# Kernel tuning notes

Measured on AMD Instinct MI355X. Metric: run time of the kernel, lower is better.

The kernel has to match this reference:

```python
import jax, jax.numpy as jnp
import numpy as np

VOCAB = 256
D = 512
L = 2
FFN = 2048
H = 8
HD = D // H  # head dim = random-feature dim m for favor+
B = 2
T = 2048


def setup_inputs() -> dict:
    key = jax.random.key(0)
    ks = jax.random.split(key, 16)
    rng = np.random.default_rng(0)

    def lin(k, fan_in, shape):
        return jax.random.normal(k, shape, jnp.float32) / np.sqrt(fan_in)

    tokens = jax.random.randint(ks[0], (B, T), 0, VOCAB)
    emb = jax.random.normal(ks[1], (VOCAB, D // 2), jnp.float32)
    Wq = lin(ks[2], D, (L, D, D)); bq = 0.01 * jax.random.normal(ks[3], (L, D), jnp.float32)
    Wk = lin(ks[4], D, (L, D, D)); bk = 0.01 * jax.random.normal(ks[5], (L, D), jnp.float32)
    Wv = lin(ks[6], D, (L, D, D)); bv = 0.01 * jax.random.normal(ks[7], (L, D), jnp.float32)
    WU = lin(ks[8], D, (L, D, FFN)); bU = 0.01 * jax.random.normal(ks[9], (L, FFN), jnp.float32)
    WV = lin(ks[10], FFN, (L, FFN, D)); bV = 0.01 * jax.random.normal(ks[11], (L, D), jnp.float32)
    Wout = lin(ks[12], D, (D, VOCAB)); bout = 0.01 * jax.random.normal(ks[13], (VOCAB,), jnp.float32)
    ln1_g = jnp.ones((L, D), jnp.float32) + 0.02 * jax.random.normal(ks[14], (L, D), jnp.float32)
    ln2_g = jnp.ones((L, D), jnp.float32) + 0.02 * jax.random.normal(ks[15], (L, D), jnp.float32)
    ln1_b = jnp.zeros((L, D), jnp.float32)
    ln2_b = jnp.zeros((L, D), jnp.float32)
    # orthogonal random features per (layer, head), scaled by sqrt(head_dim)
    rfs_np = np.stack([
        np.stack([np.linalg.qr(rng.standard_normal((HD, HD)))[0] * np.sqrt(HD) for _ in range(H)])
        for _ in range(L)
    ]).astype(np.float32)
    rfs = jnp.asarray(rfs_np)
    return dict(tokens=tokens, emb=emb, Wq=Wq, bq=bq, Wk=Wk, bk=bk, Wv=Wv, bv=bv,
                rfs=rfs, ln1_g=ln1_g, ln1_b=ln1_b, ln2_g=ln2_g, ln2_b=ln2_b,
                WU=WU, bU=bU, WV=WV, bV=bV, Wout=Wout, bout=bout)


def _layernorm(x, g, b, eps=1e-5):
    mu = jnp.mean(x, -1, keepdims=True)
    var = jnp.mean((x - mu) ** 2, -1, keepdims=True)
    return (x - mu) * jax.lax.rsqrt(var + eps) * g + b


def _favor_feat(x, rfs):
    # x: [B,T,H,d]; rfs: [H,d,m]
    xp = x * (HD ** -0.25)
    return jnp.exp(jnp.einsum('bthd,hdm->bthm', xp, rfs)
                   - 0.5 * jnp.sum(xp ** 2, -1, keepdims=True))


def _attention(x, Wq, bq, Wk, bk, Wv, bv, rfs):
    Bx, Tx, Dm = x.shape
    q = (x @ Wq + bq).reshape(Bx, Tx, H, HD)
    k = (x @ Wk + bk).reshape(Bx, Tx, H, HD)
    v = (x @ Wv + bv).reshape(Bx, Tx, H, HD)
    qf = _favor_feat(q, rfs)  # [B,T,H,m]
    kf = _favor_feat(k, rfs)
    # causal prefix-sum (num_ps / den_ps with zero init sums)
    kv_cum = jnp.cumsum(jnp.einsum('bthm,bthd->bthmd', kf, v), axis=1)
    num = jnp.einsum('bthm,bthmd->bthd', qf, kv_cum)
    den = jnp.einsum('bthm,bthm->bth', qf, jnp.cumsum(kf, axis=1))
    return (num / (den[..., None] + 1e-16)).reshape(Bx, Tx, Dm)


def _pos_embs(x):
    # x: [B,T,D//2]; concat fixed sinusoidal embeddings of size D//2
    Bx, Tx, half = x.shape
    positions = jnp.arange(Tx, dtype=x.dtype)
    freqs = jnp.exp(jnp.arange(0, half, 2, dtype=x.dtype) * (-np.log(10000.0) / half))
    args = positions[:, None] * freqs[None, :]  # [T, half//2]
    sin = jnp.broadcast_to(jnp.sin(args)[None], (Bx, Tx, args.shape[1]))
    cos = jnp.broadcast_to(jnp.cos(args)[None], (Bx, Tx, args.shape[1]))
    return jnp.concatenate([x, sin, cos], -1)


def reference(tokens, emb, Wq, bq, Wk, bk, Wv, bv, rfs,
              ln1_g, ln1_b, ln2_g, ln2_b, WU, bU, WV, bV, Wout, bout):
    x = emb[tokens]            # [B,T,D//2]
    x = _pos_embs(x)           # [B,T,D]
    for i in range(L):
        skip = x
        a = _attention(x, Wq[i], bq[i], Wk[i], bk[i], Wv[i], bv[i], rfs[i])
        a = _layernorm(a, ln1_g[i], ln1_b[i])  # on_gptln=True: LN after attention
        x = skip + a
        skip = x
        h = jax.nn.gelu(x @ WU[i] + bU[i], approximate=False)
        h = h @ WV[i] + bV[i]
        h = _layernorm(h, ln2_g[i], ln2_b[i])  # on_gptln=True: LN after FFN
        x = skip + h
    return x @ Wout + bout     # [B,T,VOCAB]
```

## Files before the change

### kernel.cpp

```cpp
#include <hip/hip_runtime.h>
#include <hip/hip_bf16.h>
#include <math.h>

#define B_  2
#define T_  2048
#define D_  512
#define H_  8
#define HD_ 64
#define FFN_ 2048
#define VOCAB_ 256
#define BT_ (B_*T_)
#define NC_ 32
#define CENT_ 4160

typedef __attribute__((ext_vector_type(8))) short short8;
typedef __attribute__((ext_vector_type(4))) float float4v;
typedef __hip_bfloat16 bf16;

__device__ __forceinline__ void load16_lds(const void* g, void* l) {
  __builtin_amdgcn_global_load_lds(
      (const __attribute__((address_space(1))) unsigned int*)g,
      (__attribute__((address_space(3))) unsigned int*)l,
      16, 0, 0);
}

__device__ __forceinline__ unsigned short f2bf(float f) {
  bf16 h = __float2bfloat16(f);
  return __builtin_bit_cast(unsigned short, h);
}
__device__ __forceinline__ float bf2f(unsigned short u) {
  unsigned int i = ((unsigned int)u) << 16;
  return __builtin_bit_cast(float, i);
}

__global__ __launch_bounds__(512) void embed_pos_kernel(
    const int* __restrict__ tokens, const float* __restrict__ emb,
    float* __restrict__ x, bf16* __restrict__ xb)
{
  int bt = blockIdx.x;
  int t  = bt & (T_ - 1);
  int j  = threadIdx.x;
  float val;
  if (j < 256) {
    int tok = tokens[bt];
    val = emb[tok * 256 + j];
  } else {
    int jj = (j - 256) & 127;
    float f = expf(-(float)(2 * jj) * (9.210340371976184f / 256.0f));
    float arg = (float)t * f;
    val = (j < 384) ? sinf(arg) : cosf(arg);
  }
  size_t off = (size_t)bt * D_ + j;
  x[off]  = val;
  xb[off] = __float2bfloat16(val);
}

__global__ __launch_bounds__(256) void prep_all_kernel(
    const float* __restrict__ Wv, const float* __restrict__ WU,
    const float* __restrict__ WVp, const float* __restrict__ Wout,
    bf16* __restrict__ WvT, bf16* __restrict__ WUT,
    bf16* __restrict__ WVT, bf16* __restrict__ WoutT,
    const float* __restrict__ bq, const float* __restrict__ bk,
    const float* __restrict__ rfs, float* __restrict__ bqf,
    float* __restrict__ bkf)
{
  __shared__ float t[32][33];
  int id = blockIdx.x;
  if (id >= 4736) {
    int z = id - 4736;
    int l = z >> 1, side = z & 1;
    const float* b = (side ? bk : bq) + l * D_;
    float* bo = (side ? bkf : bqf) + l * D_;
    for (int n = threadIdx.x; n < D_; n += 256) {
      int h = n >> 6, j = n & 63;
      const float* R = rfs + ((size_t)l * H_ + h) * 4096;
      float acc = 0.f;
      for (int d = 0; d < 64; ++d) acc += b[h * 64 + d] * R[d * 64 + j];
      bo[n] = acc * 0.35355339059327373f;
    }
    return;
  }
  const float* W; bf16* Wt; int K, N, tx, ty;
  if (id < 512) {
    int l = id >> 8, tt = id & 255;
    W = Wv + (size_t)l * D_ * D_;  Wt = WvT + (size_t)l * D_ * D_;
    K = D_; N = D_; tx = tt & 15; ty = tt >> 4;
  } else if (id < 2560) {
    int tt = id - 512; int l = tt >> 10; tt &= 1023;
    W = WU + (size_t)l * D_ * FFN_;  Wt = WUT + (size_t)l * D_ * FFN_;
    K = D_; N = FFN_; tx = tt & 63; ty = tt >> 6;
  } else if (id < 4608) {
    int tt = id - 2560; int l = tt >> 10; tt &= 1023;
    W = WVp + (size_t)l * FFN_ * D_;  Wt = WVT + (size_t)l * FFN_ * D_;
    K = FFN_; N = D_; tx = tt & 15; ty = tt >> 4;
  } else {
    int tt = id - 4608;
    W = Wout;  Wt = WoutT;
    K = D_; N = VOCAB_; tx = tt & 7; ty = tt >> 3;
  }
  int n0 = tx * 32, k0 = ty * 32;
  int lx = threadIdx.x & 31, ly = threadIdx.x >> 5;
#pragma unroll
  for (int r = 0; r < 4; ++r)
    t[ly + 8 * r][lx] = W[(size_t)(k0 + ly + 8 * r) * N + n0 + lx];
  __syncthreads();
#pragma unroll
  for (int r = 0; r < 4; ++r)
    Wt[(size_t)(n0 + ly + 8 * r) * K + k0 + lx] = __float2bfloat16(t[lx][ly + 8 * r]);
}

__global__ __launch_bounds__(256) void rf_fold_w_kernel(
    const float* __restrict__ Wq, const float* __restrict__ Wk,
    const float* __restrict__ rfs, bf16* __restrict__ WqT, bf16* __restrict__ WkT)
{
  int h = blockIdx.x, kq = blockIdx.y, z = blockIdx.z;
  int l = z >> 1, side = z & 1;
  const float* W = (side ? Wk : Wq) + (size_t)l * D_ * D_;
  bf16* WT = (side ? WkT : WqT) + (size_t)l * D_ * D_;
  const float* Rg = rfs + ((size_t)l * H_ + h) * 4096;
  __shared__ float Rl[64][65];
  __shared__ float Ws[128][65];
  int tid = threadIdx.x;
  for (int i = tid; i < 1024; i += 256) {
    float4 v4 = ((const float4*)Rg)[i];
    int d = i >> 4, j0 = (i & 15) * 4;
    Rl[d][j0] = v4.x; Rl[d][j0+1] = v4.y; Rl[d][j0+2] = v4.z; Rl[d][j0+3] = v4.w;
  }
  for (int i = tid; i < 2048; i += 256) {
    int r = i >> 4, c0 = (i & 15) * 4;
    float4 v4 = *(const float4*)&W[(size_t)(kq * 128 + r) * D_ + h * 64 + c0];
    Ws[r][c0] = v4.x; Ws[r][c0+1] = v4.y; Ws[r][c0+2] = v4.z; Ws[r][c0+3] = v4.w;
  }
  __syncthreads();
  int lane = tid & 63, w = tid >> 6;
  for (int kh = 0; kh < 2; ++kh) {
    int kk = kh * 64 + lane;
#pragma unroll 1
    for (int jj = 0; jj < 16; ++jj) {
      int j = w * 16 + jj;
      float acc = 0.f;
#pragma unroll 16
      for (int d = 0; d < 64; ++d) acc += Ws[kk][d] * Rl[d][j];
      WT[(size_t)(h * 64 + j) * D_ + kq * 128 + kk] =
          __float2bfloat16(acc * 0.35355339059327373f);
    }
  }
}

__device__ __forceinline__ void mfma_core(
    const bf16* __restrict__ A, const bf16* __restrict__ Bt,
    int strideK, int kr, int row0, int col0, float4v acc[4][4])
{
  __shared__ short Al[128 * 64];
  __shared__ short Bl[128 * 64];
  int tid = threadIdx.x;
  int lane = tid & 63, w = tid >> 6;
  int wm = (w >> 1) * 64, wn = (w & 1) * 64;
  int quad = lane >> 4, l16 = lane & 15;

  int lr = lane >> 3;
  int ks = (((lane & 7) ^ lr)) * 8;
  const short* gA[4]; const short* gB[4];
  short* lA[4]; short* lB[4];
#pragma unroll
  for (int p = 0; p < 4; ++p) {
    int r = 32 * w + 8 * p;
    gA[p] = (const short*)A + (size_t)(row0 + r + lr) * strideK + ks;
    gB[p] = (const short*)Bt + (size_t)(col0 + r + lr) * strideK + ks;
    lA[p] = Al + r * 64;
    lB[p] = Bl + r * 64;
  }
#pragma unroll
  for (int p = 0; p < 4; ++p) {
    load16_lds(gA[p], lA[p]);
    load16_lds(gB[p], lB[p]);
  }

  for (int kt = 0; kt < kr; ++kt) {
    __syncthreads();
    short8 af[4][2], bfr[4][2];
#pragma unroll
    for (int mi = 0; mi < 4; ++mi) {
      int R = wm + mi * 16 + l16;
#pragma unroll
      for (int s = 0; s < 2; ++s) {
        int slot = (s * 4 + quad) ^ (R & 7);
        af[mi][s] = *(const short8*)&Al[R * 64 + slot * 8];
      }
    }
#pragma unroll
    for (int ni = 0; ni < 4; ++ni) {
      int R = wn + ni * 16 + l16;
#pragma unroll
      for (int s = 0; s < 2; ++s) {
        int slot = (s * 4 + quad) ^ (R & 7);
        bfr[ni][s] = *(const short8*)&Bl[R * 64 + slot * 8];
      }
    }
    __syncthreads();
    if (kt + 1 < kr) {
      int o = (kt + 1) * 64;
#pragma unroll
      for (int p = 0; p < 4; ++p) {
        load16_lds(gA[p] + o, lA[p]);
        load16_lds(gB[p] + o, lB[p]);
      }
    }
#pragma unroll
    for (int mi = 0; mi < 4; ++mi)
#pragma unroll
      for (int ni = 0; ni < 4; ++ni) {
        acc[mi][ni] = __builtin_amdgcn_mfma_f32_16x16x32_bf16(
            af[mi][0], bfr[ni][0], acc[mi][ni], 0, 0, 0);
        acc[mi][ni] = __builtin_amdgcn_mfma_f32_16x16x32_bf16(
            af[mi][1], bfr[ni][1], acc[mi][ni], 0, 0, 0);
      }
  }
}

__global__ __launch_bounds__(256) void gemm_mfma(
    const bf16* __restrict__ A, const bf16* __restrict__ Bt,
    const float* __restrict__ bias, void* __restrict__ Cout,
    int M, int N, int K, int mode)
{
  int lane = threadIdx.x & 63, w = threadIdx.x >> 6;
  int wm = (w >> 1) * 64, wn = (w & 1) * 64;
  int quad = lane >> 4, l16 = lane & 15;
  int row0 = blockIdx.x * 128, col0 = blockIdx.y * 128;
  float4v acc[4][4] = {};
  mfma_core(A, Bt, K, K >> 6, row0, col0, acc);
#pragma unroll
  for (int mi = 0; mi < 4; ++mi) {
#pragma unroll
    for (int ni = 0; ni < 4; ++ni) {
      int j = col0 + wn + ni * 16 + l16;
      float bj = bias[j];
#pragma unroll
      for (int r = 0; r < 4; ++r) {
        int i = row0 + wm + mi * 16 + quad * 4 + r;
        float v = acc[mi][ni][r] + bj;
        if (mode == 1) {
          v = 0.5f * v * (1.0f + erff(v * 0.7071067811865475f));
          ((bf16*)Cout)[(size_t)i * N + j] = __float2bfloat16(v);
        } else {
          ((float*)Cout)[(size_t)i * N + j] = v;
        }
      }
    }
  }
}

__global__ __launch_bounds__(256) void gemm_qkv(
    const bf16* __restrict__ A, const bf16* __restrict__ wT,
    const float* __restrict__ bqf, const float* __restrict__ bkf,
    const float* __restrict__ bv, bf16* __restrict__ outb, int l)
{
  int z = blockIdx.z;
  const bf16* Bt = wT + ((size_t)z * 2 + l) * D_ * D_;
  const float* bias = (z == 0 ? bqf : (z == 1 ? bkf : bv)) + l * D_;
  bf16* Cout = outb + (size_t)z * BT_ * D_;
  int lane = threadIdx.x & 63, w = threadIdx.x >> 6;
  int wm = (w >> 1) * 64, wn = (w & 1) * 64;
  int quad = lane >> 4, l16 = lane & 15;
  int row0 = blockIdx.x * 128, col0 = blockIdx.y * 128;
  float4v acc[4][4] = {};
  mfma_core(A, Bt, D_, D_ >> 6, row0, col0, acc);
  if (z < 2) {
#pragma unroll
    for (int mi = 0; mi < 4; ++mi) {
      float vres[4][4];
      float sq[4] = {0.f, 0.f, 0.f, 0.f};
#pragma unroll
      for (int ni = 0; ni < 4; ++ni) {
        int j = col0 + wn + ni * 16 + l16;
        float bj = bias[j];
#pragma unroll
        for (int r = 0; r < 4; ++r) {
          float v = acc[mi][ni][r] + bj;
          vres[ni][r] = v;
          sq[r] += v * v;
        }
      }
#pragma unroll
      for (int r = 0; r < 4; ++r) {
        float s = sq[r];
        s += __shfl_xor(s, 1, 64);
        s += __shfl_xor(s, 2, 64);
        s += __shfl_xor(s, 4, 64);
        s += __shfl_xor(s, 8, 64);
        sq[r] = s;
      }
#pragma unroll
      for (int ni = 0; ni < 4; ++ni) {
        int j = col0 + wn + ni * 16 + l16;
#pragma unroll
        for (int r = 0; r < 4; ++r) {
          int i = row0 + wm + mi * 16 + quad * 4 + r;
          Cout[(size_t)i * D_ + j] =
              __float2bfloat16(__expf(vres[ni][r] - sq[r] * (1.0f / 128.0f)));
        }
      }
    }
  } else {
#pragma unroll
    for (int mi = 0; mi < 4; ++mi) {
#pragma unroll
      for (int ni = 0; ni < 4; ++ni) {
        int j = col0 + wn + ni * 16 + l16;
        float bj = bias[j];
#pragma unroll
        for (int r = 0; r < 4; ++r) {
          int i = row0 + wm + mi * 16 + quad * 4 + r;
          Cout[(size_t)i * D_ + j] = __float2bfloat16(acc[mi][ni][r] + bj);
        }
      }
    }
  }
}

__global__ __launch_bounds__(256) void gemm_splitk(
    const bf16* __restrict__ A, const bf16* __restrict__ Bt,
    float* __restrict__ P, int M, int N, int K, int KS)
{
  int s = blockIdx.z;
  int lane = threadIdx.x & 63, w = threadIdx.x >> 6;
  int wm = (w >> 1) * 64, wn = (w & 1) * 64;
  int quad = lane >> 4, l16 = lane & 15;
  int row0 = blockIdx.x * 128, col0 = blockIdx.y * 128;
  float4v acc[4][4] = {};
  mfma_core((const bf16*)((const short*)A + s * KS),
            (const bf16*)((const short*)Bt + s * KS),
            K, KS >> 6, row0, col0, acc);
  float* Ps = P + (size_t)s * M * N;
#pragma unroll
  for (int mi = 0; mi < 4; ++mi) {
#pragma unroll
    for (int ni = 0; ni < 4; ++ni) {
      int j = col0 + wn + ni * 16 + l16;
#pragma unroll
      for (int r = 0; r < 4; ++r) {
        int i = row0 + wm + mi * 16 + quad * 4 + r;
        Ps[(size_t)i * N + j] = acc[mi][ni][r];
      }
    }
  }
}

__global__ __launch_bounds__(256) void reduce4_bias_kernel(
    const float* __restrict__ P, const float* __restrict__ bias,
    float* __restrict__ C, int MN, int N)
{
  int idx = (blockIdx.x * 256 + threadIdx.x) * 4;
  float4 s0 = *(const float4*)&P[idx];
  float4 s1 = *(const float4*)&P[idx + MN];
  float4 s2 = *(const float4*)&P[idx + 2 * MN];
  float4 s3 = *(const float4*)&P[idx + 3 * MN];
  float4 b  = *(const float4*)&bias[idx & (N - 1)];
  float4 r;
  r.x = s0.x + s1.x + s2.x + s3.x + b.x;
  r.y = s0.y + s1.y + s2.y + s3.y + b.y;
  r.z = s0.z + s1.z + s2.z + s3.z + b.z;
  r.w = s0.w + s1.w + s2.w + s3.w + b.w;
  *(float4*)&C[idx] = r;
}

__global__ __launch_bounds__(256) void reduce_ln_add_kernel(
    const float* __restrict__ P, const float* __restrict__ bias,
    float* __restrict__ x, bf16* __restrict__ xb,
    const float* __restrict__ g, const float* __restrict__ bta)
{
  const int MN = BT_ * D_;
  int row = blockIdx.x;
  int tid = threadIdx.x;
  size_t base = (size_t)row * D_;
  float v0 = P[base + tid] + P[MN + base + tid] + P[2 * MN + base + tid]
           + P[3 * MN + base + tid] + bias[tid];
  float v1 = P[base + tid + 256] + P[MN + base + tid + 256]
           + P[2 * MN + base + tid + 256] + P[3 * MN + base + tid + 256]
           + bias[tid + 256];
  __shared__ float red[4];
  float w = v0 + v1;
  for (int o = 32; o > 0; o >>= 1) w += __shfl_down(w, o, 64);
  if ((tid & 63) == 0) red[tid >> 6] = w;
  __syncthreads();
  float mu = (red[0] + red[1] + red[2] + red[3]) * (1.f / 512.f);
  float d0 = v0 - mu, d1 = v1 - mu;
  __syncthreads();
  w = d0 * d0 + d1 * d1;
  for (int o = 32; o > 0; o >>= 1) w += __shfl_down(w, o, 64);
  if ((tid & 63) == 0) red[tid >> 6] = w;
  __syncthreads();
  float var = (red[0] + red[1] + red[2] + red[3]) * (1.f / 512.f);
  float rs = rsqrtf(var + 1e-5f);
  float n0 = x[base + tid]       + d0 * rs * g[tid]       + bta[tid];
  float n1 = x[base + tid + 256] + d1 * rs * g[tid + 256] + bta[tid + 256];
  x[base + tid]        = n0;
  x[base + tid + 256]  = n1;
  xb[base + tid]       = __float2bfloat16(n0);
  xb[base + tid + 256] = __float2bfloat16(n1);
}

__global__ __launch_bounds__(256) void chunk_sum_kernel(
    const bf16* __restrict__ kf, const bf16* __restrict__ vf,
    float* __restrict__ buf)
{
  int bh = blockIdx.x / 31;
  int c  = blockIdx.x % 31;
  int b = bh >> 3, h = bh & 7;
  __shared__ short KT[64 * 64];
  __shared__ short VT[64 * 64];
  __shared__ float zpart[4][64];
  int tid = threadIdx.x;
  int m = tid & 63, g = tid >> 6;
  const size_t rowbase = ((size_t)(b * T_ + c * 64)) * D_ + h * 64;
#pragma unroll
  for (int cc0 = 0; cc0 < 2; ++cc0) {
    int cc = g + cc0 * 4;
    short8 kk, vv;
#pragma unroll
    for (int u = 0; u < 8; ++u) {
      size_t off = rowbase + (size_t)(cc * 8 + u) * D_ + m;
      kk[u] = ((const short*)kf)[off];
      vv[u] = ((const short*)vf)[off];
    }
    int slot = cc ^ (m & 7);
    *(short8*)&KT[m * 64 + slot * 8] = kk;
    *(short8*)&VT[m * 64 + slot * 8] = vv;
  }
  __syncthreads();
  int quad = (tid & 63) >> 4, l16 = tid & 15;
  int ar = g * 16 + l16;
  short8 afr[2];
#pragma unroll
  for (int s = 0; s < 2; ++s)
    afr[s] = *(const short8*)&KT[ar * 64 + ((s * 4 + quad) ^ (ar & 7)) * 8];
  float4v acc[4] = {};
#pragma unroll
  for (int nd = 0; nd < 4; ++nd) {
    int br = nd * 16 + l16;
#pragma unroll
    for (int s = 0; s < 2; ++s) {
      short8 bfr = *(const short8*)&VT[br * 64 + ((s * 4 + quad) ^ (br & 7)) * 8];
      acc[nd] = __builtin_amdgcn_mfma_f32_16x16x32_bf16(afr[s], bfr, acc[nd], 0, 0, 0);
    }
  }
  float zp = 0.f;
#pragma unroll
  for (int cc0 = 0; cc0 < 2; ++cc0) {
    int cc = g + cc0 * 4;
    short8 kk = *(const short8*)&KT[m * 64 + (cc ^ (m & 7)) * 8];
#pragma unroll
    for (int u = 0; u < 8; ++u) zp += bf2f((unsigned short)kk[u]);
  }
  zpart[g][m] = zp;
  size_t bo = (size_t)(bh * 31 + c) * CENT_;
#pragma unroll
  for (int nd = 0; nd < 4; ++nd)
#pragma unroll
    for (int r = 0; r < 4; ++r)
      buf[bo + (size_t)(g * 16 + quad * 4 + r) * 64 + nd * 16 + l16] = acc[nd][r];
  __syncthreads();
  if (tid < 64)
    buf[bo + 4096 + tid] = zpart[0][tid] + zpart[1][tid] + zpart[2][tid] + zpart[3][tid];
}

__global__ __launch_bounds__(256) void chunk_prefix_kernel(float* __restrict__ buf)
{
  int bh = blockIdx.x / 17;
  int grp = blockIdx.x % 17;
  int e = grp * 256 + threadIdx.x;
  if (e >= CENT_) return;
  size_t base = (size_t)bh * 31 * CENT_ + e;
  float vals[31];
#pragma unroll
  for (int c = 0; c < 31; ++c) vals[c] = buf[base + (size_t)c * CENT_];
  float run = 0.f;
#pragma unroll
  for (int c = 0; c < 31; ++c) {
    run += vals[c];
    buf[base + (size_t)c * CENT_] = run;
  }
}

__global__ __launch_bounds__(256) void chunk_attn_kernel(
    const bf16* __restrict__ qf, const bf16* __restrict__ kf,
    const bf16* __restrict__ vf, const float* __restrict__ buf,
    float* __restrict__ out)
{
  int bh = blockIdx.x >> 5;
  int ck = blockIdx.x & 31;
  int b = bh >> 3, h = bh & 7;
  __shared__ short Qs[64 * 64];
  __shared__ short Ks[64 * 64];
  __shared__ short VT[64 * 64];
  __shared__ short S0T[64 * 64];
  __shared__ float z0[64];
  __shared__ float dlds[64];
  __shared__ float dpartA[64];
  __shared__ float dpartQ[4][64];
  int tid = threadIdx.x;
  int lane = tid & 63, w = tid >> 6;
  int quad = lane >> 4, l16 = lane & 15;
  const size_t rb = ((size_t)(b * T_ + ck * 64)) * D_ + h * 64;

  {
    int lr = lane >> 3;
    int fc = (lane & 7) ^ lr;
#pragma unroll
    for (int seg = 0; seg < 2; ++seg) {
      int r = 16 * w + 8 * seg;
      load16_lds((const short*)qf + rb + (size_t)(r + lr) * D_ + fc * 8, &Qs[r * 64]);
      load16_lds((const short*)kf + rb + (size_t)(r + lr) * D_ + fc * 8, &Ks[r * 64]);
    }
    int d = lane;
    const float* S0 = buf + (size_t)(bh * 31 + (ck > 0 ? ck - 1 : 0)) * CENT_;
#pragma unroll
    for (int cc0 = 0; cc0 < 2; ++cc0) {
      int cc = w + cc0 * 4;
      short8 vv, ss;
#pragma unroll
      for (int u = 0; u < 8; ++u) {
        vv[u] = ((const short*)vf)[rb + (size_t)(cc * 8 + u) * D_ + d];
        ss[u] = (ck > 0) ? (short)f2bf(S0[(size_t)(cc * 8 + u) * 64 + d]) : (short)0;
      }
      int slot = cc ^ (d & 7);
      *(short8*)&VT[d * 64 + slot * 8] = vv;
      *(short8*)&S0T[d * 64 + slot * 8] = ss;
    }
    if (tid < 64) z0[tid] = (ck > 0) ? S0[4096 + tid] : 0.f;
  }
  __syncthreads();

  float4v pacc[4] = {};
  {
    int ar = 16 * w + l16;
    short8 afr[2];
#pragma unroll
    for (int s = 0; s < 2; ++s)
      afr[s] = *(const short8*)&Qs[ar * 64 + ((s * 4 + quad) ^ (ar & 7)) * 8];
#pragma unroll
    for (int nj = 0; nj < 4; ++nj) {
      int br = nj * 16 + l16;
#pragma unroll
      for (int s = 0; s < 2; ++s) {
        short8 bfr = *(const short8*)&Ks[br * 64 + ((s * 4 + quad) ^ (br & 7)) * 8];
        pacc[nj] = __builtin_amdgcn_mfma_f32_16x16x32_bf16(afr[s], bfr, pacc[nj], 0, 0, 0);
      }
    }
  }
  {
    int i = lane;
    float qz = 0.f;
#pragma unroll
    for (int cc0 = 0; cc0 < 2; ++cc0) {
      int cc = w + cc0 * 4;
      short8 qq = *(const short8*)&Qs[i * 64 + (cc ^ (i & 7)) * 8];
#pragma unroll
      for (int u = 0; u < 8; ++u) qz += bf2f((unsigned short)qq[u]) * z0[cc * 8 + u];
    }
    dpartQ[w][i] = qz;
  }
  __syncthreads();

  {
    float rs[4] = {0.f, 0.f, 0.f, 0.f};
#pragma unroll
    for (int nj = 0; nj < 4; ++nj) {
#pragma unroll
      for (int r = 0; r < 4; ++r) {
        int i = 16 * w + quad * 4 + r;
        int j = nj * 16 + l16;
        float val = (j <= i) ? pacc[nj][r] : 0.f;
        rs[r] += val;
        ((unsigned short*)Ks)[i * 64 + ((j >> 3) ^ (i & 7)) * 8 + (j & 7)] = f2bf(val);
      }
    }
#pragma unroll
    for (int r = 0; r < 4; ++r) {
      float s = rs[r];
      s += __shfl_xor(s, 1, 64);
      s += __shfl_xor(s, 2, 64);
      s += __shfl_xor(s, 4, 64);
      s += __shfl_xor(s, 8, 64);
      rs[r] = s;
    }
    if (l16 == 0) {
#pragma unroll
      for (int r = 0; r < 4; ++r) dpartA[16 * w + quad * 4 + r] = rs[r];
    }
  }
  __syncthreads();
  if (tid < 64)
    dlds[tid] = dpartA[tid] + dpartQ[0][tid] + dpartQ[1][tid]
              + dpartQ[2][tid] + dpartQ[3][tid];

  float4v acc[4] = {};
  {
    int ar = 16 * w + l16;
    short8 aA[2], aQ[2];
#pragma unroll
    for (int s = 0; s < 2; ++s) {
      aA[s] = *(const short8*)&Ks[ar * 64 + ((s * 4 + quad) ^ (ar & 7)) * 8];
      aQ[s] = *(const short8*)&Qs[ar * 64 + ((s * 4 + quad) ^ (ar & 7)) * 8];
    }
#pragma unroll
    for (int nd = 0; nd < 4; ++nd) {
      int br = nd * 16 + l16;
#pragma unroll
      for (int s = 0; s < 2; ++s) {
        short8 bV = *(const short8*)&VT[br * 64 + ((s * 4 + quad) ^ (br & 7)) * 8];
        acc[nd] = __builtin_amdgcn_mfma_f32_16x16x32_bf16(aA[s], bV, acc[nd], 0, 0, 0);
        short8 bS = *(const short8*)&S0T[br * 64 + ((s * 4 + quad) ^ (br & 7)) * 8];
        acc[nd] = __builtin_amdgcn_mfma_f32_16x16x32_bf16(aQ[s], bS, acc[nd], 0, 0, 0);
      }
    }
  }
  __syncthreads();
#pragma unroll
  for (int nd = 0; nd < 4; ++nd)
#pragma unroll
    for (int r = 0; r < 4; ++r) {
      int i = 16 * w + quad * 4 + r;
      int d = nd * 16 + l16;
      out[((size_t)(b * T_ + ck * 64 + i)) * D_ + h * 64 + d] =
          acc[nd][r] / (dlds[i] + 1e-16f);
    }
}

__global__ __launch_bounds__(256) void ln_add_kernel(
    float* __restrict__ x, bf16* __restrict__ xb, const float* __restrict__ a,
    const float* __restrict__ g, const float* __restrict__ bta)
{
  int row = blockIdx.x;
  int tid = threadIdx.x;
  const float* ar = a + (size_t)row * D_;
  float v0 = ar[tid], v1 = ar[tid + 256];
  __shared__ float red[4];
  float w = v0 + v1;
  for (int o = 32; o > 0; o >>= 1) w += __shfl_down(w, o, 64);
  if ((tid & 63) == 0) red[tid >> 6] = w;
  __syncthreads();
  float mu = (red[0] + red[1] + red[2] + red[3]) * (1.f / 512.f);
  float d0 = v0 - mu, d1 = v1 - mu;
  __syncthreads();
  w = d0 * d0 + d1 * d1;
  for (int o = 32; o > 0; o >>= 1) w += __shfl_down(w, o, 64);
  if ((tid & 63) == 0) red[tid >> 6] = w;
  __syncthreads();
  float var = (red[0] + red[1] + red[2] + red[3]) * (1.f / 512.f);
  float rs = rsqrtf(var + 1e-5f);
  size_t xoff = (size_t)row * D_;
  float n0 = x[xoff + tid]       + d0 * rs * g[tid]       + bta[tid];
  float n1 = x[xoff + tid + 256] + d1 * rs * g[tid + 256] + bta[tid + 256];
  x[xoff + tid]        = n0;
  x[xoff + tid + 256]  = n1;
  xb[xoff + tid]       = __float2bfloat16(n0);
  xb[xoff + tid + 256] = __float2bfloat16(n1);
}

extern "C" void kernel_launch(void* const* d_in, const int* in_sizes, int n_in,
                              void* d_out, int out_size, void* d_ws, size_t ws_size,
                              hipStream_t stream) {
  const int*   tokens = (const int*)  d_in[0];
  const float* emb    = (const float*)d_in[1];
  const float* Wq     = (const float*)d_in[2];
  const float* bq     = (const float*)d_in[3];
  const float* Wk     = (const float*)d_in[4];
  const float* bk     = (const float*)d_in[5];
  const float* Wv     = (const float*)d_in[6];
  const float* bv     = (const float*)d_in[7];
  const float* rfs    = (const float*)d_in[8];
  const float* ln1g   = (const float*)d_in[9];
  const float* ln1b   = (const float*)d_in[10];
  const float* ln2g   = (const float*)d_in[11];
  const float* ln2b   = (const float*)d_in[12];
  const float* WU     = (const float*)d_in[13];
  const float* bU     = (const float*)d_in[14];
  const float* WV     = (const float*)d_in[15];
  const float* bV     = (const float*)d_in[16];
  const float* Wout   = (const float*)d_in[17];
  const float* bout   = (const float*)d_in[18];
  float* out = (float*)d_out;

  const size_t R = (size_t)BT_ * D_;
  float* ws = (float*)d_ws;
  float* x  = ws;
  float* ab = ws + R;
  float* sb = ws + 2 * R;
  bf16*  qb = (bf16*)(ws + 3 * R);
  bf16*  kb = (bf16*)(ws + 3 * R + R / 2);
  bf16*  vb = (bf16*)(ws + 4 * R);
  bf16*  xb = (bf16*)(ws + 4 * R + R / 2);
  bf16*  hb = (bf16*)(ws + 5 * R);
  float* pb = ws + 7 * R;
  bf16*  wT = (bf16*)(ws + 11 * R);
  bf16* WqT   = wT;
  bf16* WkT   = WqT + (size_t)2 * D_ * D_;
  bf16* WvT   = WkT + (size_t)2 * D_ * D_;
  bf16* WUT   = WvT + (size_t)2 * D_ * D_;
  bf16* WVT   = WUT + (size_t)2 * D_ * FFN_;
  bf16* WoutT = WVT + (size_t)2 * D_ * FFN_;
  float* bqf  = (float*)(WoutT + (size_t)VOCAB_ * D_);
  float* bkf  = bqf + 2 * D_;

  rf_fold_w_kernel<<<dim3(8, 4, 4), 256, 0, stream>>>(Wq, Wk, rfs, WqT, WkT);
  prep_all_kernel<<<4740, 256, 0, stream>>>(
      Wv, WU, WV, Wout, WvT, WUT, WVT, WoutT, bq, bk, rfs, bqf, bkf);

  embed_pos_kernel<<<BT_, 512, 0, stream>>>(tokens, emb, x, xb);

  for (int l = 0; l < 2; ++l) {
    gemm_qkv<<<dim3(BT_/128, D_/128, 3), 256, 0, stream>>>(
        xb, wT, bqf, bkf, bv, qb, l);

    chunk_sum_kernel<<<16 * 31, 256, 0, stream>>>(kb, vb, sb);
    chunk_prefix_kernel<<<16 * 17, 256, 0, stream>>>(sb);
    chunk_attn_kernel<<<16 * NC_, 256, 0, stream>>>(qb, kb, vb, sb, ab);

    ln_add_kernel<<<BT_, 256, 0, stream>>>(x, xb, ab, ln1g + l*D_, ln1b + l*D_);

    gemm_mfma<<<dim3(BT_/128, FFN_/128), 256, 0, stream>>>(
        xb, WUT + (size_t)l*D_*FFN_, bU + l*FFN_, hb, BT_, FFN_, D_, 1);

    gemm_splitk<<<dim3(BT_/128, D_/128, 4), 256, 0, stream>>>(
        hb, WVT + (size_t)l*FFN_*D_, pb, BT_, D_, FFN_, FFN_/4);
    reduce_ln_add_kernel<<<BT_, 256, 0, stream>>>(
        pb, bV + l*D_, x, xb, ln2g + l*D_, ln2b + l*D_);
  }

  gemm_splitk<<<dim3(BT_/128, VOCAB_/128, 4), 256, 0, stream>>>(
      xb, WoutT, pb, BT_, VOCAB_, D_, D_/4);
  reduce4_bias_kernel<<<(BT_*VOCAB_)/1024, 256, 0, stream>>>(
      pb, bout, out, BT_*VOCAB_, VOCAB_);
}
```

Before: 320.9 us.

## Merge prologue kernels into one launch and double GEMM K-tile to 128

New measurement: 354.5 us. +10.4%, slower.

```diff
diff --git a/kernel.cpp b/kernel.cpp
--- a/kernel.cpp
+++ b/kernel.cpp
@@ -33,117 +33,126 @@
   return __builtin_bit_cast(float, i);
 }
 
-__global__ __launch_bounds__(512) void embed_pos_kernel(
+__global__ __launch_bounds__(256) void prologue_kernel(
     const int* __restrict__ tokens, const float* __restrict__ emb,
-    float* __restrict__ x, bf16* __restrict__ xb)
-{
-  int bt = blockIdx.x;
-  int t  = bt & (T_ - 1);
-  int j  = threadIdx.x;
-  float val;
-  if (j < 256) {
-    int tok = tokens[bt];
-    val = emb[tok * 256 + j];
-  } else {
-    int jj = (j - 256) & 127;
-    float f = expf(-(float)(2 * jj) * (9.210340371976184f / 256.0f));
-    float arg = (float)t * f;
-    val = (j < 384) ? sinf(arg) : cosf(arg);
-  }
-  size_t off = (size_t)bt * D_ + j;
-  x[off]  = val;
-  xb[off] = __float2bfloat16(val);
-}
-
-__global__ __launch_bounds__(256) void prep_all_kernel(
+    float* __restrict__ x, bf16* __restrict__ xb,
+    const float* __restrict__ Wq, const float* __restrict__ Wk,
+    const float* __restrict__ rfs, bf16* __restrict__ WqT, bf16* __restrict__ WkT,
     const float* __restrict__ Wv, const float* __restrict__ WU,
     const float* __restrict__ WVp, const float* __restrict__ Wout,
     bf16* __restrict__ WvT, bf16* __restrict__ WUT,
     bf16* __restrict__ WVT, bf16* __restrict__ WoutT,
     const float* __restrict__ bq, const float* __restrict__ bk,
-    const float* __restrict__ rfs, float* __restrict__ bqf,
-    float* __restrict__ bkf)
-{
-  __shared__ float t[32][33];
+    float* __restrict__ bqf, float* __restrict__ bkf)
+{
+  __shared__ float sm[12480];
   int id = blockIdx.x;
-  if (id >= 4736) {
-    int z = id - 4736;
+  int tid = threadIdx.x;
+
+  if (id < 4096) {
+    int bt = id;
+    int t  = bt & (T_ - 1);
+#pragma unroll
+    for (int jj = 0; jj < 2; ++jj) {
+      int j = tid + jj * 256;
+      float val;
+      if (j < 256) {
+        int tok = tokens[bt];
+        val = emb[tok * 256 + j];
+      } else {
+        int j2 = (j - 256) & 127;
+        float f = expf(-(float)(2 * j2) * (9.210340371976184f / 256.0f));
+        float arg = (float)t * f;
+        val = (j < 384) ? sinf(arg) : cosf(arg);
+      }
+      size_t off = (size_t)bt * D_ + j;
+      x[off]  = val;
+      xb[off] = __float2bfloat16(val);
+    }
+    return;
+  }
+  if (id < 4224) {
+    int id2 = id - 4096;
+    int h = id2 & 7, kq = (id2 >> 3) & 3, z = id2 >> 5;
+    int l = z >> 1, side = z & 1;
+    const float* W = (side ? Wk : Wq) + (size_t)l * D_ * D_;
+    bf16* WT = (side ? WkT : WqT) + (size_t)l * D_ * D_;
+    const float* Rg = rfs + ((size_t)l * H_ + h) * 4096;
+    float* Rl = sm;
+    float* Ws = sm + 64 * 65;
+    for (int i = tid; i < 1024; i += 256) {
+      float4 v4 = ((const float4*)Rg)[i];
+      int d = i >> 4, j0 = (i & 15) * 4;
+      Rl[d * 65 + j0] = v4.x; Rl[d * 65 + j0 + 1] = v4.y;
+      Rl[d * 65 + j0 + 2] = v4.z; Rl[d * 65 + j0 + 3] = v4.w;
+    }
+    for (int i = tid; i < 2048; i += 256) {
+      int r = i >> 4, c0 = (i & 15) * 4;
+      float4 v4 = *(const float4*)&W[(size_t)(kq * 128 + r) * D_ + h * 64 + c0];
+      Ws[r * 65 + c0] = v4.x; Ws[r * 65 + c0 + 1] = v4.y;
+      Ws[r * 65 + c0 + 2] = v4.z; Ws[r * 65 + c0 + 3] = v4.w;
+    }
+    __syncthreads();
+    int lane = tid & 63, w = tid >> 6;
+    for (int kh = 0; kh < 2; ++kh) {
+      int kk = kh * 64 + lane;
+#pragma unroll 1
+      for (int jj = 0; jj < 16; ++jj) {
+        int j = w * 16 + jj;
+        float acc = 0.f;
+#pragma unroll 16
+        for (int d = 0; d < 64; ++d) acc += Ws[kk * 65 + d] * Rl[d * 65 + j];
+        WT[(size_t)(h * 64 + j) * D_ + kq * 128 + kk] =
+            __float2bfloat16(acc * 0.35355339059327373f);
+      }
+    }
+    return;
+  }
+  if (id < 8960) {
+    int id3 = id - 4224;
+    const float* W; bf16* Wt; int K, N, tx, ty;
+    if (id3 < 512) {
+      int l = id3 >> 8, tt = id3 & 255;
+      W = Wv + (size_t)l * D_ * D_;  Wt = WvT + (size_t)l * D_ * D_;
+      K = D_; N = D_; tx = tt & 15; ty = tt >> 4;
+    } else if (id3 < 2560) {
+      int tt = id3 - 512; int l = tt >> 10; tt &= 1023;
+      W = WU + (size_t)l * D_ * FFN_;  Wt = WUT + (size_t)l * D_ * FFN_;
+      K = D_; N = FFN_; tx = tt & 63; ty = tt >> 6;
+    } else if (id3 < 4608) {
+      int tt = id3 - 2560; int l = tt >> 10; tt &= 1023;
+      W = WVp + (size_t)l * FFN_ * D_;  Wt = WVT + (size_t)l * FFN_ * D_;
+      K = FFN_; N = D_; tx = tt & 15; ty = tt >> 4;
+    } else {
+      int tt = id3 - 4608;
+      W = Wout;  Wt = WoutT;
+      K = D_; N = VOCAB_; tx = tt & 7; ty = tt >> 3;
+    }
+    float (*tb)[33] = (float(*)[33])sm;
+    int n0 = tx * 32, k0 = ty * 32;
+    int lx = tid & 31, ly = tid >> 5;
+#pragma unroll
+    for (int r = 0; r < 4; ++r)
+      tb[ly + 8 * r][lx] = W[(size_t)(k0 + ly + 8 * r) * N + n0 + lx];
+    __syncthreads();
+#pragma unroll
+    for (int r = 0; r < 4; ++r)
+      Wt[(size_t)(n0 + ly + 8 * r) * K + k0 + lx] =
+          __float2bfloat16(tb[lx][ly + 8 * r]);
+    return;
+  }
+  {
+    int z = id - 8960;
     int l = z >> 1, side = z & 1;
     const float* b = (side ? bk : bq) + l * D_;
     float* bo = (side ? bkf : bqf) + l * D_;
-    for (int n = threadIdx.x; n < D_; n += 256) {
+    for (int n = tid; n < D_; n += 256) {
       int h = n >> 6, j = n & 63;
       const float* R = rfs + ((size_t)l * H_ + h) * 4096;
       float acc = 0.f;
       for (int d = 0; d < 64; ++d) acc += b[h * 64 + d] * R[d * 64 + j];
       bo[n] = acc * 0.35355339059327373f;
     }
-    return;
-  }
-  const float* W; bf16* Wt; int K, N, tx, ty;
-  if (id < 512) {
-    int l = id >> 8, tt = id & 255;
-    W = Wv + (size_t)l * D_ * D_;  Wt = WvT + (size_t)l * D_ * D_;
-    K = D_; N = D_; tx = tt & 15; ty = tt >> 4;
-  } else if (id < 2560) {
-    int tt = id - 512; int l = tt >> 10; tt &= 1023;
-    W = WU + (size_t)l * D_ * FFN_;  Wt = WUT + (size_t)l * D_ * FFN_;
-    K = D_; N = FFN_; tx = tt & 63; ty = tt >> 6;
-  } else if (id < 4608) {
-    int tt = id - 2560; int l = tt >> 10; tt &= 1023;
-    W = WVp + (size_t)l * FFN_ * D_;  Wt = WVT + (size_t)l * FFN_ * D_;
-    K = FFN_; N = D_; tx = tt & 15; ty = tt >> 4;
-  } else {
-    int tt = id - 4608;
-    W = Wout;  Wt = WoutT;
-    K = D_; N = VOCAB_; tx = tt & 7; ty = tt >> 3;
-  }
-  int n0 = tx * 32, k0 = ty * 32;
-  int lx = threadIdx.x & 31, ly = threadIdx.x >> 5;
-#pragma unroll
-  for (int r = 0; r < 4; ++r)
-    t[ly + 8 * r][lx] = W[(size_t)(k0 + ly + 8 * r) * N + n0 + lx];
-  __syncthreads();
-#pragma unroll
-  for (int r = 0; r < 4; ++r)
-    Wt[(size_t)(n0 + ly + 8 * r) * K + k0 + lx] = __float2bfloat16(t[lx][ly + 8 * r]);
-}
-
-__global__ __launch_bounds__(256) void rf_fold_w_kernel(
-    const float* __restrict__ Wq, const float* __restrict__ Wk,
-    const float* __restrict__ rfs, bf16* __restrict__ WqT, bf16* __restrict__ WkT)
-{
-  int h = blockIdx.x, kq = blockIdx.y, z = blockIdx.z;
-  int l = z >> 1, side = z & 1;
-  const float* W = (side ? Wk : Wq) + (size_t)l * D_ * D_;
-  bf16* WT = (side ? WkT : WqT) + (size_t)l * D_ * D_;
-  const float* Rg = rfs + ((size_t)l * H_ + h) * 4096;
-  __shared__ float Rl[64][65];
-  __shared__ float Ws[128][65];
-  int tid = threadIdx.x;
-  for (int i = tid; i < 1024; i += 256) {
-    float4 v4 = ((const float4*)Rg)[i];
-    int d = i >> 4, j0 = (i & 15) * 4;
-    Rl[d][j0] = v4.x; Rl[d][j0+1] = v4.y; Rl[d][j0+2] = v4.z; Rl[d][j0+3] = v4.w;
-  }
-  for (int i = tid; i < 2048; i += 256) {
-    int r = i >> 4, c0 = (i & 15) * 4;
-    float4 v4 = *(const float4*)&W[(size_t)(kq * 128 + r) * D_ + h * 64 + c0];
-    Ws[r][c0] = v4.x; Ws[r][c0+1] = v4.y; Ws[r][c0+2] = v4.z; Ws[r][c0+3] = v4.w;
-  }
-  __syncthreads();
-  int lane = tid & 63, w = tid >> 6;
-  for (int kh = 0; kh < 2; ++kh) {
-    int kk = kh * 64 + lane;
-#pragma unroll 1
-    for (int jj = 0; jj < 16; ++jj) {
-      int j = w * 16 + jj;
-      float acc = 0.f;
-#pragma unroll 16
-      for (int d = 0; d < 64; ++d) acc += Ws[kk][d] * Rl[d][j];
-      WT[(size_t)(h * 64 + j) * D_ + kq * 128 + kk] =
-          __float2bfloat16(acc * 0.35355339059327373f);
-    }
   }
 }
 
@@ -151,70 +160,61 @@
     const bf16* __restrict__ A, const bf16* __restrict__ Bt,
     int strideK, int kr, int row0, int col0, float4v acc[4][4])
 {
-  __shared__ short Al[128 * 64];
-  __shared__ short Bl[128 * 64];
+  __shared__ short Al[128 * 128];
+  __shared__ short Bl[128 * 128];
   int tid = threadIdx.x;
   int lane = tid & 63, w = tid >> 6;
   int wm = (w >> 1) * 64, wn = (w & 1) * 64;
   int quad = lane >> 4, l16 = lane & 15;
 
-  int lr = lane >> 3;
-  int ks = (((lane & 7) ^ lr)) * 8;
-  const short* gA[4]; const short* gB[4];
-  short* lA[4]; short* lB[4];
-#pragma unroll
-  for (int p = 0; p < 4; ++p) {
-    int r = 32 * w + 8 * p;
-    gA[p] = (const short*)A + (size_t)(row0 + r + lr) * strideK + ks;
-    gB[p] = (const short*)Bt + (size_t)(col0 + r + lr) * strideK + ks;
-    lA[p] = Al + r * 64;
-    lB[p] = Bl + r * 64;
-  }
-#pragma unroll
-  for (int p = 0; p < 4; ++p) {
-    load16_lds(gA[p], lA[p]);
-    load16_lds(gB[p], lB[p]);
+  int lr = lane >> 4, sl = lane & 15;
+  const short* gA0 = (const short*)A + (size_t)(row0 + lr) * strideK + (sl ^ lr) * 8;
+  const short* gA1 = (const short*)A + (size_t)(row0 + 4 + lr) * strideK + (sl ^ (4 + lr)) * 8;
+  const short* gB0 = (const short*)Bt + (size_t)(col0 + lr) * strideK + (sl ^ lr) * 8;
+  const short* gB1 = (const short*)Bt + (size_t)(col0 + 4 + lr) * strideK + (sl ^ (4 + lr)) * 8;
+
+#pragma unroll
+  for (int p = 0; p < 8; ++p) {
+    size_t ro = (size_t)(32 * w + (p >> 1) * 8) * strideK;
+    load16_lds(((p & 1) ? gA1 : gA0) + ro, Al + (32 * w + 4 * p) * 128);
+    load16_lds(((p & 1) ? gB1 : gB0) + ro, Bl + (32 * w + 4 * p) * 128);
   }
 
   for (int kt = 0; kt < kr; ++kt) {
     __syncthreads();
-    short8 af[4][2], bfr[4][2];
+    short8 af[4][4], bfr[4][4];
 #pragma unroll
     for (int mi = 0; mi < 4; ++mi) {
       int R = wm + mi * 16 + l16;
 #pragma unroll
-      for (int s = 0; s < 2; ++s) {
-        int slot = (s * 4 + quad) ^ (R & 7);
-        af[mi][s] = *(const short8*)&Al[R * 64 + slot * 8];
-      }
+      for (int s = 0; s < 4; ++s)
+        af[mi][s] = *(const short8*)&Al[R * 128 + ((4 * s + quad) ^ (R & 7)) * 8];
     }
 #pragma unroll
     for (int ni = 0; ni < 4; ++ni) {
       int R = wn + ni * 16 + l16;
 #pragma unroll
-      for (int s = 0; s < 2; ++s) {
-        int slot = (s * 4 + quad) ^ (R & 7);
-        bfr[ni][s] = *(const short8*)&Bl[R * 64 + slot * 8];
-      }
+      for (int s = 0; s < 4; ++s)
+        bfr[ni][s] = *(const short8*)&Bl[R * 128 + ((4 * s + quad) ^ (R & 7)) * 8];
     }
     __syncthreads();
     if (kt + 1 < kr) {
-      int o = (kt + 1) * 64;
-#pragma unroll
-      for (int p = 0; p < 4; ++p) {
-        load16_lds(gA[p] + o, lA[p]);
-        load16_lds(gB[p] + o, lB[p]);
-      }
-    }
-#pragma unroll
-    for (int mi = 0; mi < 4; ++mi)
-#pragma unroll
-      for (int ni = 0; ni < 4; ++ni) {
-        acc[mi][ni] = __builtin_amdgcn_mfma_f32_16x16x32_bf16(
-            af[mi][0], bfr[ni][0], acc[mi][ni], 0, 0, 0);
-        acc[mi][ni] = __builtin_amdgcn_mfma_f32_16x16x32_bf16(
-            af[mi][1], bfr[ni][1], acc[mi][ni], 0, 0, 0);
-      }
+      int o = (kt + 1) * 128;
+#pragma unroll
+      for (int p = 0; p < 8; ++p) {
+        size_t ro = (size_t)(32 * w + (p >> 1) * 8) * strideK + o;
+        load16_lds(((p & 1) ? gA1 : gA0) + ro, Al + (32 * w + 4 * p) * 128);
+        load16_lds(((p & 1) ? gB1 : gB0) + ro, Bl + (32 * w + 4 * p) * 128);
+      }
+    }
+#pragma unroll
+    for (int s = 0; s < 4; ++s)
+#pragma unroll
+      for (int mi = 0; mi < 4; ++mi)
+#pragma unroll
+        for (int ni = 0; ni < 4; ++ni)
+          acc[mi][ni] = __builtin_amdgcn_mfma_f32_16x16x32_bf16(
+              af[mi][s], bfr[ni][s], acc[mi][ni], 0, 0, 0);
   }
 }
 
@@ -228,7 +228,7 @@
   int quad = lane >> 4, l16 = lane & 15;
   int row0 = blockIdx.x * 128, col0 = blockIdx.y * 128;
   float4v acc[4][4] = {};
-  mfma_core(A, Bt, K, K >> 6, row0, col0, acc);
+  mfma_core(A, Bt, K, K >> 7, row0, col0, acc);
 #pragma unroll
   for (int mi = 0; mi < 4; ++mi) {
 #pragma unroll
@@ -264,7 +264,7 @@
   int quad = lane >> 4, l16 = lane & 15;
   int row0 = blockIdx.x * 128, col0 = blockIdx.y * 128;
   float4v acc[4][4] = {};
-  mfma_core(A, Bt, D_, D_ >> 6, row0, col0, acc);
+  mfma_core(A, Bt, D_, D_ >> 7, row0, col0, acc);
   if (z < 2) {
 #pragma unroll
     for (int mi = 0; mi < 4; ++mi) {
@@ -330,7 +330,7 @@
   float4v acc[4][4] = {};
   mfma_core((const bf16*)((const short*)A + s * KS),
             (const bf16*)((const short*)Bt + s * KS),
-            K, KS >> 6, row0, col0, acc);
+            K, KS >> 7, row0, col0, acc);
   float* Ps = P + (size_t)s * M * N;
 #pragma unroll
   for (int mi = 0; mi < 4; ++mi) {
@@ -703,11 +703,9 @@
   float* bqf  = (float*)(WoutT + (size_t)VOCAB_ * D_);
   float* bkf  = bqf + 2 * D_;
 
-  rf_fold_w_kernel<<<dim3(8, 4, 4), 256, 0, stream>>>(Wq, Wk, rfs, WqT, WkT);
-  prep_all_kernel<<<4740, 256, 0, stream>>>(
-      Wv, WU, WV, Wout, WvT, WUT, WVT, WoutT, bq, bk, rfs, bqf, bkf);
-
-  embed_pos_kernel<<<BT_, 512, 0, stream>>>(tokens, emb, x, xb);
+  prologue_kernel<<<8964, 256, 0, stream>>>(
+      tokens, emb, x, xb, Wq, Wk, rfs, WqT, WkT,
+      Wv, WU, WV, Wout, WvT, WUT, WVT, WoutT, bq, bk, bqf, bkf);
 
   for (int l = 0; l < 2; ++l) {
     gemm_qkv<<<dim3(BT_/128, D_/128, 3), 256, 0, stream>>>(
```
